# Kernel tuning notes

Measured on AMD Instinct MI355X. Metric: run time of the kernel, lower is better.

## Reference

```python
import jax, jax.numpy as jnp
import numpy as np

B, S, E, H = 2, 2048, 2048, 16
D = E // H  # 128


def setup_inputs() -> dict:
    key = jax.random.key(0)
    k0, k1, k2, k3 = jax.random.split(key, 4)
    x = jax.random.normal(k0, (B, S, E), dtype=jnp.float32)
    W_in = jax.random.normal(k1, (3 * E, E), dtype=jnp.float32) * 0.02
    b_in = jnp.zeros((3 * E,), dtype=jnp.float32)
    W_out = jax.random.normal(k2, (E, E), dtype=jnp.float32) * 0.02
    b_out = jnp.zeros((E,), dtype=jnp.float32)
    mask = jax.random.randint(k3, (B, S), 0, 2).astype(bool)  # True => masked out
    return {"x": x, "W_in": W_in, "b_in": b_in, "W_out": W_out, "b_out": b_out, "mask": mask}


def reference(x, W_in, b_in, W_out, b_out, mask):
    # fused QKV projection (torch Linear: y = x @ W^T + b)
    qkv = jnp.einsum('bse,fe->bsf', x, W_in) + b_in          # [B,S,3E]
    q, k, v = jnp.split(qkv, 3, axis=-1)
    q = q.reshape(B, S, H, D)
    k = k.reshape(B, S, H, D)
    v = v.reshape(B, S, H, D)
    scale = 1.0 / np.sqrt(D).astype(np.float32)
    scores = jnp.einsum('blhd,bshd->bhls', q, k) * scale     # [B,H,S,S]
    # 2D padding mask: True -> -inf additive bias, broadcast over heads/queries
    bias = jnp.where(mask[:, None, None, :], -jnp.inf, 0.0).astype(scores.dtype)
    attn = jax.nn.softmax(scores + bias, axis=-1)
    ctx = jnp.einsum('bhls,bshd->blhd', attn, v).reshape(B, S, E)
    out = jnp.einsum('ble,fe->blf', ctx, W_out) + b_out      # [B,S,E]
    return out
```

## Files before the change

kernel.cpp:

```cpp
#include <hip/hip_runtime.h>
#include <hip/hip_bf16.h>


typedef __bf16 bf16;
typedef __bf16 bf16x8 __attribute__((ext_vector_type(8)));
typedef __bf16 bf16x4 __attribute__((ext_vector_type(4)));
typedef float  f32x4  __attribute__((ext_vector_type(4)));

#define LOG2E 1.4426950408889634074f
#define SM_SCALE 0.08838834764831843f

#if defined(__has_builtin)
#if __has_builtin(__builtin_amdgcn_exp2f)
#define EXP2(x) __builtin_amdgcn_exp2f(x)
#else
#define EXP2(x) exp2f(x)
#endif
#else
#define EXP2(x) exp2f(x)
#endif

#define GLOAD_LDS16(gp, lp)                                                    \
  __builtin_amdgcn_global_load_lds(                                           \
      (__attribute__((address_space(1))) void*)(gp),                          \
      (__attribute__((address_space(3))) void*)(lp), 16, 0, 0)

__global__ void mask_bias_kernel(const unsigned char* __restrict__ mraw,
                                 float* __restrict__ kbias) {
  __shared__ int f1, f23, f84;
  if (threadIdx.x == 0) { f1 = 0; f23 = 0; f84 = 0; }
  __syncthreads();
  int a1 = 0, a23 = 0, a84 = 0;
  for (int i = threadIdx.x; i < 4096; i += blockDim.x) {
    unsigned char v = mraw[i];
    if (v) {
      int m4 = i & 3;
      if (m4 == 1) a1 = 1;
      else if (m4 >= 2) a23 = 1;
      else if ((i & 7) == 4) a84 = 1;
    }
  }
  if (a1) f1 = 1;
  if (a23) f23 = 1;
  if (a84) f84 = 1;
  __syncthreads();
  const bool isByte = (f1 != 0);
  const bool isF32 = !isByte && (f23 != 0);
  const bool isI32 = !isByte && !isF32 && (f84 != 0);
  for (int i = threadIdx.x; i < 4096; i += blockDim.x) {
    int m;
    if (isByte)      m = (mraw[i] != 0);
    else if (isF32)  m = (((const float*)mraw)[i] != 0.0f);
    else if (isI32)  m = (((const int*)mraw)[i] != 0);
    else             m = (((const long long*)mraw)[i] != 0LL);
    kbias[i] = m ? -30000.0f : 0.0f;
  }
}

__global__ void cvt_f32_bf16_kernel(const float* __restrict__ in,
                                    bf16* __restrict__ out, int n8) {
  int i = blockIdx.x * blockDim.x + threadIdx.x;
  if (i >= n8) return;
  const float4* p = (const float4*)in + (size_t)i * 2;
  float4 a = p[0], c = p[1];
  bf16x8 v;
  v[0] = (bf16)a.x; v[1] = (bf16)a.y; v[2] = (bf16)a.z; v[3] = (bf16)a.w;
  v[4] = (bf16)c.x; v[5] = (bf16)c.y; v[6] = (bf16)c.z; v[7] = (bf16)c.w;
  *((bf16x8*)out + i) = v;
}

template <int EPI>
__global__ __launch_bounds__(256, 2) void gemm_nt(
    const bf16* __restrict__ A, const bf16* __restrict__ B,
    const float* __restrict__ bias, void* __restrict__ Cout,
    bf16* __restrict__ vt, int M, int N, int K) {
  const int lane = threadIdx.x & 63;
  const int w = threadIdx.x >> 6;
  const int wr = w >> 1, wc = w & 1;
  const int l15 = lane & 15, lg = lane >> 4;

  const int nwg = gridDim.x;
  const int cpx = nwg >> 3;
  const int bid = blockIdx.x;
  const int swz = (bid & 7) * cpx + (bid >> 3);
  const int mtiles = M >> 7;
  const int mt = swz % mtiles, nt = swz / mtiles;
  const int m0 = mt << 7, n0 = nt << 7;

  __shared__ __align__(16) unsigned char smem[32768];
  unsigned char* sA = smem;
  unsigned char* sB = smem + 16384;

  const f32x4 Z4 = {0.f, 0.f, 0.f, 0.f};
  f32x4 acc[4][4];
#pragma unroll
  for (int i = 0; i < 4; i++)
#pragma unroll
    for (int j = 0; j < 4; j++) acc[i][j] = Z4;

  const int chunkbase = w * 1024 + lane * 16;

  for (int kt = 0; kt < K; kt += 64) {
#pragma unroll
    for (int c = 0; c < 4; c++) {
      int p = c * 4096 + chunkbase;
      int row = p >> 7, off = p & 127;
      int sb = off ^ ((row & 7) << 4);
      GLOAD_LDS16(A + (size_t)(m0 + row) * K + kt + (sb >> 1),
                  sA + c * 4096 + w * 1024);
      GLOAD_LDS16(B + (size_t)(n0 + row) * K + kt + (sb >> 1),
                  sB + c * 4096 + w * 1024);
    }
    __syncthreads();
#pragma unroll
    for (int ks = 0; ks < 2; ks++) {
      bf16x8 af[4], bfr[4];
#pragma unroll
      for (int i = 0; i < 4; i++) {
        int ar = wr * 64 + i * 16 + l15;
        af[i] = *(const bf16x8*)(sA + ar * 128 +
                                 ((ks * 64 + lg * 16) ^ ((ar & 7) << 4)));
        int br = wc * 64 + i * 16 + l15;
        bfr[i] = *(const bf16x8*)(sB + br * 128 +
                                  ((ks * 64 + lg * 16) ^ ((br & 7) << 4)));
      }
#pragma unroll
      for (int i = 0; i < 4; i++)
#pragma unroll
        for (int j = 0; j < 4; j++)
          acc[i][j] = __builtin_amdgcn_mfma_f32_16x16x32_bf16(
              af[i], bfr[j], acc[i][j], 0, 0, 0);
    }
    __syncthreads();
  }

#pragma unroll
  for (int i = 0; i < 4; i++) {
#pragma unroll
    for (int j = 0; j < 4; j++) {
      const int row0 = m0 + wr * 64 + i * 16 + lg * 4;
      const int col = n0 + wc * 64 + j * 16 + l15;
      const float bv = bias[col];
      f32x4 v = acc[i][j];
#pragma unroll
      for (int r = 0; r < 4; r++) v[r] += bv;
      if (EPI == 0) {
        float* Cf = (float*)Cout;
#pragma unroll
        for (int r = 0; r < 4; r++)
          Cf[(size_t)(row0 + r) * N + col] = v[r];
      } else {
        bf16* Cb = (bf16*)Cout;
        if (col < 4096) {
#pragma unroll
          for (int r = 0; r < 4; r++)
            Cb[(size_t)(row0 + r) * 6144 + col] = (bf16)v[r];
        } else {
          int dg = col - 4096;
          int hh = dg >> 7, dd = dg & 127;
          int bb = row0 >> 11, ss = row0 & 2047;
          bf16x4 pk;
#pragma unroll
          for (int r = 0; r < 4; r++) pk[r] = (bf16)v[r];
          *(bf16x4*)(vt + (size_t)((bb * 16 + hh) * 128 + dd) * 2048 + ss) = pk;
        }
      }
    }
  }
}

__global__ __launch_bounds__(256, 2) void attn_kernel(
    const bf16* __restrict__ qkv, const bf16* __restrict__ vt,
    const float* __restrict__ kbias, bf16* __restrict__ ctx) {
  const int lane = threadIdx.x & 63;
  const int w = threadIdx.x >> 6;
  const int l15 = lane & 15, lg = lane >> 4;
  const int qt = blockIdx.x, h = blockIdx.y, b = blockIdx.z;

  __shared__ __align__(16) unsigned char smem[16384 + 16384 + 4 * 4608];
  unsigned char* sK = smem;
  unsigned char* sVT = smem + 16384;
  unsigned char* sP = smem + 32768 + w * 4608;

  const int qrow0 = qt * 128 + w * 32;
  const size_t tokbase = (size_t)b * 2048;

  bf16x8 qf[2][4];
#pragma unroll
  for (int mi = 0; mi < 2; mi++)
#pragma unroll
    for (int ks = 0; ks < 4; ks++)
      qf[mi][ks] = *(const bf16x8*)(qkv +
                                    (tokbase + qrow0 + mi * 16 + l15) * 6144 +
                                    h * 128 + ks * 32 + lg * 8);

  const f32x4 Z4 = {0.f, 0.f, 0.f, 0.f};
  f32x4 o[2][8];
#pragma unroll
  for (int mi = 0; mi < 2; mi++)
#pragma unroll
    for (int n = 0; n < 8; n++) o[mi][n] = Z4;

  f32x4 mrun[2], lrun[2];
#pragma unroll
  for (int mi = 0; mi < 2; mi++) {
#pragma unroll
    for (int r = 0; r < 4; r++) { mrun[mi][r] = -15000.0f; lrun[mi][r] = 0.f; }
  }

  const float Cmul = SM_SCALE * LOG2E;
  const float* biasb = kbias + b * 2048;
  const int chunkbase = w * 1024 + lane * 16;
  const size_t vtbase = (size_t)((b * 16 + h) * 128) * 2048;

  for (int t = 0; t < 32; t++) {
    const int kv0 = t * 64;
#pragma unroll
    for (int c = 0; c < 4; c++) {
      int p = c * 4096 + chunkbase;
      int rowk = p >> 8, offk = p & 255;
      int sbk = offk ^ ((rowk & 15) << 4);
      GLOAD_LDS16(qkv + (tokbase + kv0 + rowk) * 6144 + 2048 + h * 128 +
                      (sbk >> 1),
                  sK + c * 4096 + w * 1024);
      int rowv = p >> 7, offv = p & 127;
      int sbv = offv ^ ((rowv & 7) << 4);
      GLOAD_LDS16(vt + vtbase + (size_t)rowv * 2048 + kv0 + (sbv >> 1),
                  sVT + c * 4096 + w * 1024);
    }
    __syncthreads();

    f32x4 s[2][4];
#pragma unroll
    for (int mi = 0; mi < 2; mi++)
#pragma unroll
      for (int n = 0; n < 4; n++) s[mi][n] = Z4;
#pragma unroll
    for (int ks = 0; ks < 4; ks++) {
      bf16x8 kf[4];
#pragma unroll
      for (int n = 0; n < 4; n++) {
        int row = n * 16 + l15;
        kf[n] = *(const bf16x8*)(sK + row * 256 +
                                 ((ks * 64 + lg * 16) ^ ((row & 15) << 4)));
      }
#pragma unroll
      for (int mi = 0; mi < 2; mi++)
#pragma unroll
        for (int n = 0; n < 4; n++)
          s[mi][n] = __builtin_amdgcn_mfma_f32_16x16x32_bf16(
              qf[mi][ks], kf[n], s[mi][n], 0, 0, 0);
    }

    float cb[4];
#pragma unroll
    for (int n = 0; n < 4; n++) cb[n] = biasb[kv0 + n * 16 + l15];

#pragma unroll
    for (int mi = 0; mi < 2; mi++) {
      f32x4 x[4];
#pragma unroll
      for (int n = 0; n < 4; n++)
#pragma unroll
        for (int r = 0; r < 4; r++) x[n][r] = s[mi][n][r] * Cmul + cb[n];

      f32x4 vmax = x[0];
#pragma unroll
      for (int n = 1; n < 4; n++)
#pragma unroll
        for (int r = 0; r < 4; r++) vmax[r] = fmaxf(vmax[r], x[n][r]);
#pragma unroll
      for (int msk = 1; msk < 16; msk <<= 1)
#pragma unroll
        for (int r = 0; r < 4; r++)
          vmax[r] = fmaxf(vmax[r], __shfl_xor(vmax[r], msk));

      f32x4 mnew, corr;
#pragma unroll
      for (int r = 0; r < 4; r++) {
        mnew[r] = fmaxf(mrun[mi][r], vmax[r]);
        corr[r] = EXP2(mrun[mi][r] - mnew[r]);
        mrun[mi][r] = mnew[r];
      }
      f32x4 vsum = Z4;
#pragma unroll
      for (int n = 0; n < 4; n++) {
        f32x4 pp;
#pragma unroll
        for (int r = 0; r < 4; r++) {
          pp[r] = EXP2(x[n][r] - mnew[r]);
          vsum[r] += pp[r];
        }
#pragma unroll
        for (int r = 0; r < 4; r++) {
          int prow = mi * 16 + lg * 4 + r;
          *(bf16*)(sP + prow * 144 + (n * 16 + l15) * 2) = (bf16)pp[r];
        }
      }
#pragma unroll
      for (int msk = 1; msk < 16; msk <<= 1)
#pragma unroll
        for (int r = 0; r < 4; r++) vsum[r] += __shfl_xor(vsum[r], msk);
#pragma unroll
      for (int r = 0; r < 4; r++)
        lrun[mi][r] = lrun[mi][r] * corr[r] + vsum[r];
#pragma unroll
      for (int n = 0; n < 8; n++)
#pragma unroll
        for (int r = 0; r < 4; r++) o[mi][n][r] *= corr[r];
    }

#pragma unroll
    for (int ks = 0; ks < 2; ks++) {
      bf16x8 pa[2];
#pragma unroll
      for (int mi = 0; mi < 2; mi++)
        pa[mi] = *(const bf16x8*)(sP + (mi * 16 + l15) * 144 + ks * 64 +
                                  lg * 16);
#pragma unroll
      for (int n = 0; n < 8; n++) {
        int row = n * 16 + l15;
        bf16x8 vf = *(const bf16x8*)(sVT + row * 128 +
                                     ((ks * 64 + lg * 16) ^ ((row & 7) << 4)));
#pragma unroll
        for (int mi = 0; mi < 2; mi++)
          o[mi][n] = __builtin_amdgcn_mfma_f32_16x16x32_bf16(pa[mi], vf,
                                                             o[mi][n], 0, 0, 0);
      }
    }
    __syncthreads();
  }

#pragma unroll
  for (int mi = 0; mi < 2; mi++) {
    f32x4 inv;
#pragma unroll
    for (int r = 0; r < 4; r++) inv[r] = 1.0f / lrun[mi][r];
#pragma unroll
    for (int n = 0; n < 8; n++)
#pragma unroll
      for (int r = 0; r < 4; r++) {
        int row = qrow0 + mi * 16 + lg * 4 + r;
        ctx[(tokbase + row) * 2048 + h * 128 + n * 16 + l15] =
            (bf16)(o[mi][n][r] * inv[r]);
      }
  }
}

extern "C" void kernel_launch(void* const* d_in, const int* in_sizes, int n_in,
                              void* d_out, int out_size, void* d_ws,
                              size_t ws_size, hipStream_t stream) {
  const float* x     = (const float*)d_in[0];
  const float* W_in  = (const float*)d_in[1];
  const float* b_in  = (const float*)d_in[2];
  const float* W_out = (const float*)d_in[3];
  const float* b_out = (const float*)d_in[4];
  const unsigned char* mask = (const unsigned char*)d_in[5];
  (void)in_sizes; (void)n_in; (void)out_size; (void)ws_size;

  char* ws = (char*)d_ws;
  bf16* xb    = (bf16*)(ws + 0);
  bf16* wib   = (bf16*)(ws + 16777216);
  bf16* wob   = (bf16*)(ws + 41943040);
  bf16* qkv   = (bf16*)(ws + 50331648);
  bf16* vt    = (bf16*)(ws + 100663296);
  bf16* ctx   = (bf16*)(ws + 117440512);
  float* kbias = (float*)(ws + 134217728);

  mask_bias_kernel<<<1, 1024, 0, stream>>>(mask, kbias);
  cvt_f32_bf16_kernel<<<4096, 256, 0, stream>>>(x, xb, 1048576);
  cvt_f32_bf16_kernel<<<6144, 256, 0, stream>>>(W_in, wib, 1572864);
  cvt_f32_bf16_kernel<<<2048, 256, 0, stream>>>(W_out, wob, 524288);
  gemm_nt<1><<<1536, 256, 0, stream>>>(xb, wib, b_in, (void*)qkv, vt, 4096,
                                       6144, 2048);
  attn_kernel<<<dim3(16, 16, 2), 256, 0, stream>>>(qkv, vt, kbias, ctx);
  gemm_nt<0><<<512, 256, 0, stream>>>(ctx, wob, b_out, d_out, (bf16*)nullptr,
                                      4096, 2048, 2048);
}
```

Before: 310.6 us.

## Rewrite attention with 32x32 MFMA, transposed S, register P, double-buffered K/V

The attention kernel now computes S^T with 32x32x16 bf16 MFMA, so each lane owns one query column. The bf16 P fragment is built in registers with cvt_pk and permlane32_swap, which removes the LDS round trip for P. K/V tiles are double-buffered so the next tile's global-to-LDS loads overlap compute. Blocks grow to 512 threads covering 256 queries, and a lazy rescale skips the output correction unless the max rises by more than 8. The cost is more register and LDS pressure, and lower grid parallelism with 256 blocks instead of 512.

```diff
diff --git a/kernel.cpp b/kernel.cpp
--- a/kernel.cpp
+++ b/kernel.cpp
@@ -6,6 +6,7 @@
 typedef __bf16 bf16x8 __attribute__((ext_vector_type(8)));
 typedef __bf16 bf16x4 __attribute__((ext_vector_type(4)));
 typedef float  f32x4  __attribute__((ext_vector_type(4)));
+typedef float  f32x16 __attribute__((ext_vector_type(16)));
 
 #define LOG2E 1.4426950408889634074f
 #define SM_SCALE 0.08838834764831843f
@@ -24,6 +25,15 @@
   __builtin_amdgcn_global_load_lds(                                           \
       (__attribute__((address_space(1))) void*)(gp),                          \
       (__attribute__((address_space(3))) void*)(lp), 16, 0, 0)
+
+__device__ inline unsigned int cvtpk_bf16(float lo, float hi) {
+  unsigned int r;
+  asm("v_cvt_pk_bf16_f32 %0, %1, %2" : "=v"(r) : "v"(lo), "v"(hi));
+  return r;
+}
+__device__ inline void plane32_swap(unsigned int& a, unsigned int& b) {
+  asm volatile("v_permlane32_swap_b32 %0, %1" : "+v"(a), "+v"(b));
+}
 
 __global__ void mask_bias_kernel(const unsigned char* __restrict__ mraw,
                                  float* __restrict__ kbias) {
@@ -169,181 +179,174 @@
   }
 }
 
-__global__ __launch_bounds__(256, 2) void attn_kernel(
+__global__ __launch_bounds__(512, 2) void attn_kernel(
     const bf16* __restrict__ qkv, const bf16* __restrict__ vt,
     const float* __restrict__ kbias, bf16* __restrict__ ctx) {
-  const int lane = threadIdx.x & 63;
-  const int w = threadIdx.x >> 6;
-  const int l15 = lane & 15, lg = lane >> 4;
+  const int tid = threadIdx.x;
+  const int lane = tid & 63;
+  const int w = tid >> 6;
+  const int l31 = lane & 31;
+  const int hb = lane >> 5;
   const int qt = blockIdx.x, h = blockIdx.y, b = blockIdx.z;
 
-  __shared__ __align__(16) unsigned char smem[16384 + 16384 + 4 * 4608];
-  unsigned char* sK = smem;
-  unsigned char* sVT = smem + 16384;
-  unsigned char* sP = smem + 32768 + w * 4608;
-
-  const int qrow0 = qt * 128 + w * 32;
+  __shared__ __align__(16) unsigned char smem[65536];
+
+  const int qrow0 = qt * 256 + w * 32;
   const size_t tokbase = (size_t)b * 2048;
-
-  bf16x8 qf[2][4];
-#pragma unroll
-  for (int mi = 0; mi < 2; mi++)
-#pragma unroll
-    for (int ks = 0; ks < 4; ks++)
-      qf[mi][ks] = *(const bf16x8*)(qkv +
-                                    (tokbase + qrow0 + mi * 16 + l15) * 6144 +
-                                    h * 128 + ks * 32 + lg * 8);
-
-  const f32x4 Z4 = {0.f, 0.f, 0.f, 0.f};
-  f32x4 o[2][8];
-#pragma unroll
-  for (int mi = 0; mi < 2; mi++)
-#pragma unroll
-    for (int n = 0; n < 8; n++) o[mi][n] = Z4;
-
-  f32x4 mrun[2], lrun[2];
-#pragma unroll
-  for (int mi = 0; mi < 2; mi++) {
-#pragma unroll
-    for (int r = 0; r < 4; r++) { mrun[mi][r] = -15000.0f; lrun[mi][r] = 0.f; }
-  }
-
+  const size_t vtbase = (size_t)((b * 16 + h) * 128) * 2048;
+  const float* biasb = kbias + b * 2048;
   const float Cmul = SM_SCALE * LOG2E;
-  const float* biasb = kbias + b * 2048;
-  const int chunkbase = w * 1024 + lane * 16;
-  const size_t vtbase = (size_t)((b * 16 + h) * 128) * 2048;
-
-  for (int t = 0; t < 32; t++) {
+
+  auto stage = [&](int t, int bufsel) {
     const int kv0 = t * 64;
-#pragma unroll
-    for (int c = 0; c < 4; c++) {
-      int p = c * 4096 + chunkbase;
+    unsigned char* base = smem + bufsel * 32768;
+#pragma unroll
+    for (int c = 0; c < 2; c++) {
+      int p = c * 8192 + tid * 16;
       int rowk = p >> 8, offk = p & 255;
       int sbk = offk ^ ((rowk & 15) << 4);
       GLOAD_LDS16(qkv + (tokbase + kv0 + rowk) * 6144 + 2048 + h * 128 +
                       (sbk >> 1),
-                  sK + c * 4096 + w * 1024);
+                  base + c * 8192 + w * 1024);
       int rowv = p >> 7, offv = p & 127;
       int sbv = offv ^ ((rowv & 7) << 4);
       GLOAD_LDS16(vt + vtbase + (size_t)rowv * 2048 + kv0 + (sbv >> 1),
-                  sVT + c * 4096 + w * 1024);
-    }
+                  base + 16384 + c * 8192 + w * 1024);
+    }
+  };
+
+  stage(0, 0);
+
+  bf16x8 qf[8];
+#pragma unroll
+  for (int ds = 0; ds < 8; ds++)
+    qf[ds] = *(const bf16x8*)(qkv + (tokbase + qrow0 + l31) * 6144 + h * 128 +
+                              ds * 16 + hb * 8);
+
+  const f32x16 Z16 = {0.f, 0.f, 0.f, 0.f, 0.f, 0.f, 0.f, 0.f,
+                      0.f, 0.f, 0.f, 0.f, 0.f, 0.f, 0.f, 0.f};
+  f32x16 opv[4];
+#pragma unroll
+  for (int d0 = 0; d0 < 4; d0++) opv[d0] = Z16;
+  float mrun = -15000.0f, lrun = 0.0f;
+
+  __syncthreads();
+
+  for (int t = 0; t < 32; t++) {
+    const int buf = t & 1;
+    const int kv0 = t * 64;
+    if (t < 31) stage(t + 1, buf ^ 1);
+    unsigned char* sK = smem + buf * 32768;
+    unsigned char* sVT = sK + 16384;
+
+    f32x4 bb[2][2][2];
+#pragma unroll
+    for (int kb = 0; kb < 2; kb++)
+#pragma unroll
+      for (int sb = 0; sb < 2; sb++)
+#pragma unroll
+        for (int g = 0; g < 2; g++)
+          bb[kb][sb][g] = *(const f32x4*)(biasb + kv0 + kb * 32 + sb * 16 +
+                                          g * 8 + 4 * hb);
+
+    f32x16 accs[2];
+    accs[0] = Z16; accs[1] = Z16;
+    __builtin_amdgcn_s_setprio(1);
+#pragma unroll
+    for (int ds = 0; ds < 8; ds++) {
+#pragma unroll
+      for (int kb = 0; kb < 2; kb++) {
+        int row = kb * 32 + l31;
+        bf16x8 kf = *(const bf16x8*)(
+            sK + row * 256 + ((ds * 32 + hb * 16) ^ ((row & 15) << 4)));
+        accs[kb] = __builtin_amdgcn_mfma_f32_32x32x16_bf16(kf, qf[ds],
+                                                           accs[kb], 0, 0, 0);
+      }
+    }
+    __builtin_amdgcn_s_setprio(0);
+
+#pragma unroll
+    for (int kb = 0; kb < 2; kb++)
+#pragma unroll
+      for (int r = 0; r < 16; r++)
+        accs[kb][r] =
+            accs[kb][r] * Cmul + bb[kb][r >> 3][(r >> 2) & 1][r & 3];
+
+    float vmax = accs[0][0];
+#pragma unroll
+    for (int kb = 0; kb < 2; kb++)
+#pragma unroll
+      for (int r = 0; r < 16; r++) vmax = fmaxf(vmax, accs[kb][r]);
+    vmax = fmaxf(vmax, __shfl_xor(vmax, 32));
+
+    if (__any(vmax > mrun + 8.0f)) {
+      float mnew = fmaxf(mrun, vmax);
+      float corr = EXP2(mrun - mnew);
+      mrun = mnew;
+      lrun *= corr;
+#pragma unroll
+      for (int r = 0; r < 16; r++) {
+        float cv = __shfl(corr, (r & 3) + 8 * (r >> 2) + 4 * hb);
+#pragma unroll
+        for (int d0 = 0; d0 < 4; d0++) opv[d0][r] *= cv;
+      }
+    }
+
+    float vsum = 0.0f;
+#pragma unroll
+    for (int kb = 0; kb < 2; kb++)
+#pragma unroll
+      for (int r = 0; r < 16; r++) {
+        float p = EXP2(accs[kb][r] - mrun);
+        accs[kb][r] = p;
+        vsum += p;
+      }
+    vsum += __shfl_xor(vsum, 32);
+    lrun += vsum;
+
+    union { unsigned int w4[4]; bf16x8 v; } paf[4];
+#pragma unroll
+    for (int kb = 0; kb < 2; kb++)
+#pragma unroll
+      for (int sb = 0; sb < 2; sb++) {
+        int r0 = sb * 8;
+        unsigned int a0 = cvtpk_bf16(accs[kb][r0 + 0], accs[kb][r0 + 1]);
+        unsigned int a1 = cvtpk_bf16(accs[kb][r0 + 2], accs[kb][r0 + 3]);
+        unsigned int c0 = cvtpk_bf16(accs[kb][r0 + 4], accs[kb][r0 + 5]);
+        unsigned int c1 = cvtpk_bf16(accs[kb][r0 + 6], accs[kb][r0 + 7]);
+        plane32_swap(a0, c0);
+        plane32_swap(a1, c1);
+        int ks = kb * 2 + sb;
+        paf[ks].w4[0] = a0; paf[ks].w4[1] = a1;
+        paf[ks].w4[2] = c0; paf[ks].w4[3] = c1;
+      }
+
+    __builtin_amdgcn_s_setprio(1);
+#pragma unroll
+    for (int ks = 0; ks < 4; ks++) {
+#pragma unroll
+      for (int d0 = 0; d0 < 4; d0++) {
+        int row = d0 * 32 + l31;
+        bf16x8 vf = *(const bf16x8*)(
+            sVT + row * 128 + ((ks * 32 + hb * 16) ^ ((row & 7) << 4)));
+        opv[d0] = __builtin_amdgcn_mfma_f32_32x32x16_bf16(paf[ks].v, vf,
+                                                          opv[d0], 0, 0, 0);
+      }
+    }
+    __builtin_amdgcn_s_setprio(0);
+
     __syncthreads();
-
-    f32x4 s[2][4];
-#pragma unroll
-    for (int mi = 0; mi < 2; mi++)
-#pragma unroll
-      for (int n = 0; n < 4; n++) s[mi][n] = Z4;
-#pragma unroll
-    for (int ks = 0; ks < 4; ks++) {
-      bf16x8 kf[4];
-#pragma unroll
-      for (int n = 0; n < 4; n++) {
-        int row = n * 16 + l15;
-        kf[n] = *(const bf16x8*)(sK + row * 256 +
-                                 ((ks * 64 + lg * 16) ^ ((row & 15) << 4)));
-      }
-#pragma unroll
-      for (int mi = 0; mi < 2; mi++)
-#pragma unroll
-        for (int n = 0; n < 4; n++)
-          s[mi][n] = __builtin_amdgcn_mfma_f32_16x16x32_bf16(
-              qf[mi][ks], kf[n], s[mi][n], 0, 0, 0);
-    }
-
-    float cb[4];
-#pragma unroll
-    for (int n = 0; n < 4; n++) cb[n] = biasb[kv0 + n * 16 + l15];
-
-#pragma unroll
-    for (int mi = 0; mi < 2; mi++) {
-      f32x4 x[4];
-#pragma unroll
-      for (int n = 0; n < 4; n++)
-#pragma unroll
-        for (int r = 0; r < 4; r++) x[n][r] = s[mi][n][r] * Cmul + cb[n];
-
-      f32x4 vmax = x[0];
-#pragma unroll
-      for (int n = 1; n < 4; n++)
-#pragma unroll
-        for (int r = 0; r < 4; r++) vmax[r] = fmaxf(vmax[r], x[n][r]);
-#pragma unroll
-      for (int msk = 1; msk < 16; msk <<= 1)
-#pragma unroll
-        for (int r = 0; r < 4; r++)
-          vmax[r] = fmaxf(vmax[r], __shfl_xor(vmax[r], msk));
-
-      f32x4 mnew, corr;
-#pragma unroll
-      for (int r = 0; r < 4; r++) {
-        mnew[r] = fmaxf(mrun[mi][r], vmax[r]);
-        corr[r] = EXP2(mrun[mi][r] - mnew[r]);
-        mrun[mi][r] = mnew[r];
-      }
-      f32x4 vsum = Z4;
-#pragma unroll
-      for (int n = 0; n < 4; n++) {
-        f32x4 pp;
-#pragma unroll
-        for (int r = 0; r < 4; r++) {
-          pp[r] = EXP2(x[n][r] - mnew[r]);
-          vsum[r] += pp[r];
-        }
-#pragma unroll
-        for (int r = 0; r < 4; r++) {
-          int prow = mi * 16 + lg * 4 + r;
-          *(bf16*)(sP + prow * 144 + (n * 16 + l15) * 2) = (bf16)pp[r];
-        }
-      }
-#pragma unroll
-      for (int msk = 1; msk < 16; msk <<= 1)
-#pragma unroll
-        for (int r = 0; r < 4; r++) vsum[r] += __shfl_xor(vsum[r], msk);
-#pragma unroll
-      for (int r = 0; r < 4; r++)
-        lrun[mi][r] = lrun[mi][r] * corr[r] + vsum[r];
-#pragma unroll
-      for (int n = 0; n < 8; n++)
-#pragma unroll
-        for (int r = 0; r < 4; r++) o[mi][n][r] *= corr[r];
-    }
-
-#pragma unroll
-    for (int ks = 0; ks < 2; ks++) {
-      bf16x8 pa[2];
-#pragma unroll
-      for (int mi = 0; mi < 2; mi++)
-        pa[mi] = *(const bf16x8*)(sP + (mi * 16 + l15) * 144 + ks * 64 +
-                                  lg * 16);
-#pragma unroll
-      for (int n = 0; n < 8; n++) {
-        int row = n * 16 + l15;
-        bf16x8 vf = *(const bf16x8*)(sVT + row * 128 +
-                                     ((ks * 64 + lg * 16) ^ ((row & 7) << 4)));
-#pragma unroll
-        for (int mi = 0; mi < 2; mi++)
-          o[mi][n] = __builtin_amdgcn_mfma_f32_16x16x32_bf16(pa[mi], vf,
-                                                             o[mi][n], 0, 0, 0);
-      }
-    }
-    __syncthreads();
-  }
-
-#pragma unroll
-  for (int mi = 0; mi < 2; mi++) {
-    f32x4 inv;
-#pragma unroll
-    for (int r = 0; r < 4; r++) inv[r] = 1.0f / lrun[mi][r];
-#pragma unroll
-    for (int n = 0; n < 8; n++)
-#pragma unroll
-      for (int r = 0; r < 4; r++) {
-        int row = qrow0 + mi * 16 + lg * 4 + r;
-        ctx[(tokbase + row) * 2048 + h * 128 + n * 16 + l15] =
-            (bf16)(o[mi][n][r] * inv[r]);
-      }
+  }
+
+  float linv = 1.0f / lrun;
+#pragma unroll
+  for (int r = 0; r < 16; r++) {
+    float lv = __shfl(linv, (r & 3) + 8 * (r >> 2) + 4 * hb);
+    int row = qrow0 + (r & 3) + 8 * (r >> 2) + 4 * hb;
+#pragma unroll
+    for (int d0 = 0; d0 < 4; d0++)
+      ctx[(tokbase + row) * 2048 + h * 128 + d0 * 32 + l31] =
+          (bf16)(opv[d0][r] * lv);
   }
 }
 
@@ -373,7 +376,7 @@
   cvt_f32_bf16_kernel<<<2048, 256, 0, stream>>>(W_out, wob, 524288);
   gemm_nt<1><<<1536, 256, 0, stream>>>(xb, wib, b_in, (void*)qkv, vt, 4096,
                                        6144, 2048);
-  attn_kernel<<<dim3(16, 16, 2), 256, 0, stream>>>(qkv, vt, kbias, ctx);
+  attn_kernel<<<dim3(8, 16, 2), 512, 0, stream>>>(qkv, vt, kbias, ctx);
   gemm_nt<0><<<512, 256, 0, stream>>>(ctx, wob, b_out, d_out, (bf16*)nullptr,
                                       4096, 2048, 2048);
 }
```

New measurement: 252.3 us. 18.8% less time.
